# Performance work log

Measured on AMD Instinct MI355X. Metric: run time of the kernel, lower is better.

Reference implementation:

```python
import jax, jax.numpy as jnp
import numpy as np

D_MODEL, D_FF, N_EXPERTS, TOP_K = 512, 2048, 8, 2


def setup_inputs() -> dict:
    key = jax.random.key(0)
    ks = jax.random.split(key, 7)
    B, S = 2, 2048
    x = jax.random.normal(ks[0], (B, S, D_MODEL), dtype=jnp.float32)
    s1 = 1.0 / np.sqrt(D_MODEL)
    s2 = 1.0 / np.sqrt(D_FF)
    Wg = jax.random.normal(ks[1], (D_MODEL, N_EXPERTS), dtype=jnp.float32) * s1
    bg = jnp.zeros((N_EXPERTS,), dtype=jnp.float32)
    W1 = jax.random.normal(ks[2], (N_EXPERTS, D_MODEL, D_FF), dtype=jnp.float32) * s1
    b1 = jax.random.normal(ks[3], (N_EXPERTS, D_FF), dtype=jnp.float32) * s1
    W2 = jax.random.normal(ks[4], (N_EXPERTS, D_FF, D_MODEL), dtype=jnp.float32) * s2
    b2 = jax.random.normal(ks[5], (N_EXPERTS, D_MODEL), dtype=jnp.float32) * s2
    return {"x": x, "Wg": Wg, "bg": bg, "W1": W1, "b1": b1, "W2": W2, "b2": b2}


def reference(x, Wg, bg, W1, b1, W2, b2):
    B, S, D = x.shape
    xt = x.reshape(B * S, D)  # [T, D]
    # gating
    gate_logits = xt @ Wg + bg                      # [T, E]
    gate_scores = jax.nn.softmax(gate_logits, axis=-1)
    topk_scores, topk_idx = jax.lax.top_k(gate_scores, TOP_K)  # [T, K]
    topk_scores = topk_scores / jnp.sum(topk_scores, axis=-1, keepdims=True)
    # combine weights per expert: [T, E]
    combine = jnp.sum(jax.nn.one_hot(topk_idx, N_EXPERTS, dtype=xt.dtype)
                      * topk_scores[..., None], axis=1)
    # dense per-expert MLP (exact GELU, dropout is identity in eval)
    h = jax.nn.gelu(jnp.einsum('td,edf->etf', xt, W1) + b1[:, None, :],
                    approximate=False)             # [E, T, F]
    expert_out = jnp.einsum('etf,efd->etd', h, W2) + b2[:, None, :]  # [E, T, D]
    out = jnp.einsum('te,etd->td', combine, expert_out)
    return out.reshape(B, S, D)
```

## Files before the change

kernel.cpp:

```cpp
#include <hip/hip_runtime.h>
#include <hip/hip_bf16.h>
#include <math.h>

#define D_MODEL 512
#define D_FF    2048
#define NEXP    8

using bf16x8 = __attribute__((ext_vector_type(8))) short;
using f32x4  = __attribute__((ext_vector_type(4))) float;

__device__ inline unsigned short f2bf(float x) {
    __hip_bfloat16 h = __float2bfloat16(x);
    unsigned short u; __builtin_memcpy(&u, &h, 2); return u;
}
__device__ inline unsigned pk(float a, float b) {
    return (unsigned)f2bf(a) | ((unsigned)f2bf(b) << 16);
}
__device__ inline float erf_fast(float x) {
    float ax = fabsf(x);
    float t  = 1.f / fmaf(0.3275911f, ax, 1.f);
    float p  = t * fmaf(t, fmaf(t, fmaf(t, fmaf(t, 1.061405429f, -1.453152027f),
                                        1.421413741f), -0.284496736f), 0.254829592f);
    float r  = 1.f - p * __expf(-ax * ax);
    return copysignf(r, x);
}
__device__ inline float gelu_exact(float v) {
    return 0.5f * v * (1.f + erf_fast(v * 0.70710678118654752f));
}
__device__ inline void gload_lds16(const void* g, void* l) {
    __builtin_amdgcn_global_load_lds(
        (const __attribute__((address_space(1))) unsigned int*)g,
        (__attribute__((address_space(3))) unsigned int*)l, 16, 0, 0);
}

__global__ __launch_bounds__(256) void gate_kernel(
    const float* __restrict__ x, const float* __restrict__ Wg,
    const float* __restrict__ bg,
    int2* __restrict__ tk_e, float2* __restrict__ tk_s,
    unsigned short* __restrict__ Xb, int T)
{
    int lane = threadIdx.x & 63;
    int w    = threadIdx.x >> 6;
    int t    = blockIdx.x * 4 + w;
    if (t >= T) return;

    const float* xr = x + (size_t)t * D_MODEL;
    unsigned short* xbr = Xb ? (Xb + (size_t)t * D_MODEL) : nullptr;
    float lg[NEXP];
#pragma unroll
    for (int e = 0; e < NEXP; e++) lg[e] = 0.f;

#pragma unroll
    for (int it = 0; it < D_MODEL / 64; it++) {
        int d = lane + 64 * it;
        float xv = xr[d];
        if (xbr) xbr[d] = f2bf(xv);
        const float* wr = Wg + (size_t)d * NEXP;
#pragma unroll
        for (int e = 0; e < NEXP; e++) lg[e] += xv * wr[e];
    }
#pragma unroll
    for (int off = 32; off > 0; off >>= 1) {
#pragma unroll
        for (int e = 0; e < NEXP; e++) lg[e] += __shfl_xor(lg[e], off, 64);
    }

    if (lane == 0) {
#pragma unroll
        for (int e = 0; e < NEXP; e++) lg[e] += bg[e];
        int e0 = 0;
#pragma unroll
        for (int e = 1; e < NEXP; e++) if (lg[e] > lg[e0]) e0 = e;
        int e1 = (e0 == 0) ? 1 : 0;
#pragma unroll
        for (int e = 0; e < NEXP; e++) if (e != e0 && lg[e] > lg[e1]) e1 = e;
        float s0 = 1.f / (1.f + expf(lg[e1] - lg[e0]));
        tk_e[t] = make_int2(e0, e1);
        tk_s[t] = make_float2(s0, 1.f - s0);
    }
}

__global__ __launch_bounds__(256) void route_kernel(
    const int2* __restrict__ tk_e, const float2* __restrict__ tk_s,
    int* __restrict__ counts, int* __restrict__ ltok, float* __restrict__ lsc,
    int2* __restrict__ tk_pos, int T)
{
    int t    = blockIdx.x * 256 + threadIdx.x;
    int lane = threadIdx.x & 63;
    bool valid = t < T;
    int2   es = valid ? tk_e[t] : make_int2(-1, -1);
    float2 ss = valid ? tk_s[t] : make_float2(0.f, 0.f);
    int ppos[2] = {0, 0};

#pragma unroll
    for (int slot = 0; slot < 2; slot++) {
        int   e = slot ? es.y : es.x;
        float s = slot ? ss.y : ss.x;
#pragma unroll
        for (int ex = 0; ex < NEXP; ex++) {
            unsigned long long m = __ballot(e == ex);
            if (m == 0ull) continue;
            int leader = __ffsll((long long)m) - 1;
            int base = 0;
            if (lane == leader) base = atomicAdd(&counts[ex], __popcll(m));
            base = __shfl(base, leader, 64);
            if (e == ex) {
                int pos = base + __popcll(m & ((1ull << lane) - 1ull));
                ltok[(size_t)ex * T + pos] = t;
                lsc [(size_t)ex * T + pos] = s;
                ppos[slot] = pos | (ex << 16);
            }
        }
    }
    if (valid) tk_pos[t] = make_int2(ppos[0], ppos[1]);
}

__global__ void prefix_kernel(const int* __restrict__ counts, int* __restrict__ offs)
{
    if (threadIdx.x == 0) {
        int acc = 0;
        for (int e = 0; e < NEXP; e++) { offs[e] = acc; acc += counts[e]; }
        offs[NEXP] = acc;
    }
}

__global__ __launch_bounds__(256) void tcvt_kernel(
    const float* __restrict__ src, unsigned short* __restrict__ dst, int R, int C)
{
    __shared__ unsigned short tile[64][72];
    int e  = blockIdx.z;
    int r0 = blockIdx.y * 64, c0 = blockIdx.x * 64;
    const float* s = src + ((size_t)e * R + r0) * C + c0;
    unsigned short* d = dst + ((size_t)e * C + c0) * R + r0;
    int t = threadIdx.x;
#pragma unroll
    for (int i = 0; i < 4; i++) {
        int idx = t + 256 * i;
        int r = idx >> 4, c4 = (idx & 15) * 4;
        float4 v = *(const float4*)(s + (size_t)r * C + c4);
        tile[c4    ][r] = f2bf(v.x);
        tile[c4 + 1][r] = f2bf(v.y);
        tile[c4 + 2][r] = f2bf(v.z);
        tile[c4 + 3][r] = f2bf(v.w);
    }
    __syncthreads();
#pragma unroll
    for (int i = 0; i < 2; i++) {
        int idx = t + 256 * i;
        int c = idx >> 3, q = idx & 7;
        uint4 v = *(const uint4*)(&tile[c][q * 8]);
        *(uint4*)(d + (size_t)c * R + q * 8) = v;
    }
}

__global__ __launch_bounds__(512, 4) void moe_gemm1(
    const unsigned short* __restrict__ Xb,
    const unsigned short* __restrict__ W1t, const float* __restrict__ b1,
    const int* __restrict__ counts, const int* __restrict__ offs,
    const int* __restrict__ ltok,
    unsigned short* __restrict__ Hg, int T)
{
    int e = blockIdx.x;
    int n = counts[e];
    int mbase = blockIdx.y * 128;
    if (mbase >= n) return;
    int fb = blockIdx.z * 128;
    int off = offs[e];

    __shared__ __align__(16) unsigned char SB[2][16384];
    __shared__ int toks_s[128];

    int tid = threadIdx.x, lane = tid & 63, wid = tid >> 6;
    int wr = wid & 3, wc = wid >> 2;

    if (tid < 128) {
        int idx = mbase + tid; if (idx > n - 1) idx = n - 1;
        toks_s[tid] = ltok[(size_t)e * T + idx];
    }
    __syncthreads();

    const unsigned short* W1te = W1t + (size_t)e * D_FF * D_MODEL;
    int c = lane & 7, rsub = lane >> 3;

    const char* aptr[2]; const char* bptr[2]; int soff[2];
#pragma unroll
    for (int j = 0; j < 2; j++) {
        int r  = j * 64 + wid * 8 + rsub;
        int sc = c ^ (r & 7);
        aptr[j] = (const char*)(Xb + (size_t)toks_s[r] * D_MODEL) + sc * 16;
        bptr[j] = (const char*)(W1te + (size_t)(fb + r) * D_MODEL) + sc * 16;
        soff[j] = (j * 64 + wid * 8) * 128;
    }

    f32x4 acc[2][4];
#pragma unroll
    for (int i = 0; i < 2; i++)
#pragma unroll
        for (int j = 0; j < 4; j++) acc[i][j] = (f32x4){0.f, 0.f, 0.f, 0.f};

    for (int kc = 0; kc < D_MODEL; kc += 64) {
#pragma unroll
        for (int j = 0; j < 2; j++) gload_lds16(aptr[j] + kc * 2, SB[0] + soff[j]);
#pragma unroll
        for (int j = 0; j < 2; j++) gload_lds16(bptr[j] + kc * 2, SB[1] + soff[j]);
        __syncthreads();

#pragma unroll
        for (int ks = 0; ks < 2; ks++) {
            bf16x8 av[2], bv[4];
            int kbyte = ks * 64 + ((lane >> 4) * 16);
#pragma unroll
            for (int i = 0; i < 2; i++) {
                int row = wr * 32 + i * 16 + (lane & 15);
                av[i] = *(const bf16x8*)(SB[0] + row * 128 + (kbyte ^ ((row & 7) << 4)));
            }
#pragma unroll
            for (int j = 0; j < 4; j++) {
                int fr = wc * 64 + j * 16 + (lane & 15);
                bv[j] = *(const bf16x8*)(SB[1] + fr * 128 + (kbyte ^ ((fr & 7) << 4)));
            }
#pragma unroll
            for (int i = 0; i < 2; i++)
#pragma unroll
                for (int j = 0; j < 4; j++)
                    acc[i][j] = __builtin_amdgcn_mfma_f32_16x16x32_bf16(av[i], bv[j], acc[i][j], 0, 0, 0);
        }
        __syncthreads();
    }

    char* Eb = (char*)&SB[0][0];
    const float* b1e = b1 + (size_t)e * D_FF;
#pragma unroll
    for (int j = 0; j < 4; j++) {
        int col = wc * 64 + j * 16 + (lane & 15);
        float b1v = b1e[fb + col];
#pragma unroll
        for (int i = 0; i < 2; i++) {
#pragma unroll
            for (int r = 0; r < 4; r++) {
                int row = wr * 32 + i * 16 + (lane >> 4) * 4 + r;
                float v = gelu_exact(acc[i][j][r] + b1v);
                *(unsigned short*)(Eb + row * 256 + ((col * 2) ^ ((row & 7) << 4))) = f2bf(v);
            }
        }
    }
    __syncthreads();
#pragma unroll
    for (int k = 0; k < 4; k++) {
        int idx = tid + 512 * k;
        int row = idx >> 4, ch = idx & 15;
        if (mbase + row < n) {
            uint4 v = *(const uint4*)(Eb + row * 256 + ((ch * 16) ^ ((row & 7) << 4)));
            *(uint4*)(Hg + (size_t)(off + mbase + row) * D_FF + fb + ch * 8) = v;
        }
    }
}

__global__ __launch_bounds__(512, 4) void moe_gemm2_og(
    const unsigned short* __restrict__ Hg,
    const unsigned short* __restrict__ W2t, const float* __restrict__ b2,
    const int* __restrict__ counts, const int* __restrict__ offs,
    const int* __restrict__ ltok, const float* __restrict__ lsc,
    float* __restrict__ Og, int T)
{
    int e = blockIdx.x;
    int n = counts[e];
    int mbase = blockIdx.y * 128;
    if (mbase >= n) return;
    int nb = blockIdx.z & 3, kb = blockIdx.z >> 2;
    int db = nb * 128;
    int off = offs[e];

    __shared__ __align__(16) unsigned char SB[2][16384];
    __shared__ float scs_s[128];

    int tid = threadIdx.x, lane = tid & 63, wid = tid >> 6;
    int wr = wid & 3, wc = wid >> 2;

    if (tid < 128) {
        int idx = mbase + tid; if (idx > n - 1) idx = n - 1;
        scs_s[tid] = lsc[(size_t)e * T + idx];
    }
    __syncthreads();

    const unsigned short* W2te = W2t + (size_t)e * D_MODEL * D_FF;
    int c = lane & 7, rsub = lane >> 3;

    const char* aptr[2]; const char* bptr[2]; int soff[2];
#pragma unroll
    for (int j = 0; j < 2; j++) {
        int r = j * 64 + wid * 8 + rsub;
        int srow = mbase + r; if (srow > n - 1) srow = n - 1;
        int sc = c ^ (r & 7);
        aptr[j] = (const char*)(Hg + (size_t)(off + srow) * D_FF) + sc * 16;
        bptr[j] = (const char*)(W2te + (size_t)(db + r) * D_FF) + sc * 16;
        soff[j] = (j * 64 + wid * 8) * 128;
    }

    f32x4 acc[2][4];
#pragma unroll
    for (int i = 0; i < 2; i++)
#pragma unroll
        for (int j = 0; j < 4; j++) acc[i][j] = (f32x4){0.f, 0.f, 0.f, 0.f};

    int kbase = kb * 1024;
    for (int kc = 0; kc < 1024; kc += 64) {
        int kabs = kbase + kc;
#pragma unroll
        for (int j = 0; j < 2; j++) gload_lds16(aptr[j] + kabs * 2, SB[0] + soff[j]);
#pragma unroll
        for (int j = 0; j < 2; j++) gload_lds16(bptr[j] + kabs * 2, SB[1] + soff[j]);
        __syncthreads();

#pragma unroll
        for (int ks = 0; ks < 2; ks++) {
            bf16x8 av[2], bv[4];
            int kbyte = ks * 64 + ((lane >> 4) * 16);
#pragma unroll
            for (int i = 0; i < 2; i++) {
                int row = wr * 32 + i * 16 + (lane & 15);
                av[i] = *(const bf16x8*)(SB[0] + row * 128 + (kbyte ^ ((row & 7) << 4)));
            }
#pragma unroll
            for (int j = 0; j < 4; j++) {
                int dr = wc * 64 + j * 16 + (lane & 15);
                bv[j] = *(const bf16x8*)(SB[1] + dr * 128 + (kbyte ^ ((dr & 7) << 4)));
            }
#pragma unroll
            for (int i = 0; i < 2; i++)
#pragma unroll
                for (int j = 0; j < 4; j++)
                    acc[i][j] = __builtin_amdgcn_mfma_f32_16x16x32_bf16(av[i], bv[j], acc[i][j], 0, 0, 0);
        }
        __syncthreads();
    }

    float* Ogk = Og + (size_t)kb * (2 * T) * D_MODEL;
#pragma unroll
    for (int j = 0; j < 4; j++) {
        int dg = db + wc * 64 + j * 16 + (lane & 15);
        float b2v = (kb == 0) ? b2[(size_t)e * D_MODEL + dg] : 0.f;
#pragma unroll
        for (int i = 0; i < 2; i++) {
#pragma unroll
            for (int r = 0; r < 4; r++) {
                int rowm = wr * 32 + i * 16 + (lane >> 4) * 4 + r;
                if (mbase + rowm < n) {
                    float s = scs_s[rowm];
                    Ogk[(size_t)(off + mbase + rowm) * D_MODEL + dg] = s * (acc[i][j][r] + b2v);
                }
            }
        }
    }
}

__global__ __launch_bounds__(256) void combine_kernel(
    const float* __restrict__ Og, const int* __restrict__ offs,
    const int2* __restrict__ tk_pos, float* __restrict__ out, int T)
{
    int w = threadIdx.x >> 6, lane = threadIdx.x & 63;
    int t = blockIdx.x * 4 + w;
    if (t >= T) return;
    int2 p = tk_pos[t];
    int sA = offs[p.x >> 16] + (p.x & 0xffff);
    int sB = offs[p.y >> 16] + (p.y & 0xffff);
    size_t S = (size_t)(2 * T) * D_MODEL;
    const float4* r0 = (const float4*)(Og + (size_t)sA * D_MODEL);
    const float4* r1 = (const float4*)(Og + S + (size_t)sA * D_MODEL);
    const float4* r2 = (const float4*)(Og + (size_t)sB * D_MODEL);
    const float4* r3 = (const float4*)(Og + S + (size_t)sB * D_MODEL);
    float4* o = (float4*)(out + (size_t)t * D_MODEL);
#pragma unroll
    for (int i = 0; i < 2; i++) {
        int idx = lane + 64 * i;
        float4 a = r0[idx], b = r1[idx], cc = r2[idx], d = r3[idx];
        o[idx] = make_float4(a.x + b.x + cc.x + d.x, a.y + b.y + cc.y + d.y,
                             a.z + b.z + cc.z + d.z, a.w + b.w + cc.w + d.w);
    }
}

__global__ __launch_bounds__(256, 4) void moe_gemm2(
    const unsigned short* __restrict__ Hg,
    const unsigned short* __restrict__ W2t, const float* __restrict__ b2,
    const int* __restrict__ counts, const int* __restrict__ offs,
    const int* __restrict__ ltok, const float* __restrict__ lsc,
    float* __restrict__ out, int T)
{
    int e = blockIdx.x;
    int n = counts[e];
    int mbase = blockIdx.y * 128;
    if (mbase >= n) return;
    int nb = blockIdx.z & 3, kb = blockIdx.z >> 2;
    int db = nb * 128;
    int off = offs[e];

    __shared__ __align__(16) unsigned char HsB[128 * 128];
    __shared__ __align__(16) unsigned char WsB[128 * 128];
    __shared__ int   toks_s[128];
    __shared__ float scs_s[128];

    int tid = threadIdx.x, lane = tid & 63, w = tid >> 6;
    int wr = w & 1, wc = w >> 1;

    if (tid < 128) {
        int idx = mbase + tid; if (idx > n - 1) idx = n - 1;
        toks_s[tid] = ltok[(size_t)e * T + idx];
        scs_s [tid] = lsc [(size_t)e * T + idx];
    }
    __syncthreads();

    const unsigned short* W2te = W2t + (size_t)e * D_MODEL * D_FF;
    int c = lane & 7, rsub = lane >> 3;

    const char* aptr[4]; const char* bptr[4]; int soff[4];
#pragma unroll
    for (int j = 0; j < 4; j++) {
        int r = j * 32 + w * 8 + rsub;
        int srow = mbase + r; if (srow > n - 1) srow = n - 1;
        int sc = c ^ (r & 7);
        aptr[j] = (const char*)(Hg + (size_t)(off + srow) * D_FF) + sc * 16;
        bptr[j] = (const char*)(W2te + (size_t)(db + r) * D_FF) + sc * 16;
        soff[j] = (j * 32 + w * 8) * 128;
    }

    f32x4 acc[4][4];
#pragma unroll
    for (int i = 0; i < 4; i++)
#pragma unroll
        for (int j = 0; j < 4; j++) acc[i][j] = (f32x4){0.f, 0.f, 0.f, 0.f};

    int kbase = kb * 1024;
    for (int kc = 0; kc < 1024; kc += 64) {
        int kabs = kbase + kc;
#pragma unroll
        for (int j = 0; j < 4; j++) gload_lds16(aptr[j] + kabs * 2, HsB + soff[j]);
#pragma unroll
        for (int j = 0; j < 4; j++) gload_lds16(bptr[j] + kabs * 2, WsB + soff[j]);
        __syncthreads();

#pragma unroll
        for (int ks = 0; ks < 2; ks++) {
            bf16x8 av[4], bv[4];
            int kbyte = ks * 64 + ((lane >> 4) * 16);
#pragma unroll
            for (int i = 0; i < 4; i++) {
                int row = wr * 64 + i * 16 + (lane & 15);
                av[i] = *(const bf16x8*)(HsB + row * 128 + (kbyte ^ ((row & 7) << 4)));
            }
#pragma unroll
            for (int j = 0; j < 4; j++) {
                int dr = wc * 64 + j * 16 + (lane & 15);
                bv[j] = *(const bf16x8*)(WsB + dr * 128 + (kbyte ^ ((dr & 7) << 4)));
            }
#pragma unroll
            for (int i = 0; i < 4; i++)
#pragma unroll
                for (int j = 0; j < 4; j++)
                    acc[i][j] = __builtin_amdgcn_mfma_f32_16x16x32_bf16(av[i], bv[j], acc[i][j], 0, 0, 0);
        }
        __syncthreads();
    }

#pragma unroll
    for (int j = 0; j < 4; j++) {
        int dg = db + wc * 64 + j * 16 + (lane & 15);
        float b2v = (kb == 0) ? b2[(size_t)e * D_MODEL + dg] : 0.f;
#pragma unroll
        for (int i = 0; i < 4; i++) {
#pragma unroll
            for (int r = 0; r < 4; r++) {
                int rowm = wr * 64 + i * 16 + (lane >> 4) * 4 + r;
                if (mbase + rowm < n) {
                    float s = scs_s[rowm];
                    int tok = toks_s[rowm];
                    atomicAdd(out + (size_t)tok * D_MODEL + dg, s * (acc[i][j][r] + b2v));
                }
            }
        }
    }
}

__global__ __launch_bounds__(512, 2) void moe_gemm1_rs(
    const float* __restrict__ x,
    const float* __restrict__ W1, const float* __restrict__ b1,
    const int* __restrict__ counts, const int* __restrict__ offs,
    const int* __restrict__ ltok,
    unsigned short* __restrict__ Hg, int T)
{
    int e = blockIdx.x;
    int n = counts[e];
    int mbase = blockIdx.y * 128;
    if (mbase >= n) return;
    int fb = blockIdx.z * 256;
    int off = offs[e];

    __shared__ __align__(16) unsigned char XsB[128 * 128];
    __shared__ __align__(16) unsigned char WtB[256 * 128];
    __shared__ int toks_s[128];

    int tid  = threadIdx.x;
    int lane = tid & 63;
    int w    = tid >> 6;
    int wr   = w & 1, wc = w >> 1;

    if (tid < 128) {
        int idx = mbase + tid; if (idx > n - 1) idx = n - 1;
        toks_s[tid] = ltok[(size_t)e * T + idx];
    }
    __syncthreads();

    const float* W1e = W1 + (size_t)e * D_MODEL * D_FF;

    f32x4 acc[4][4];
#pragma unroll
    for (int i = 0; i < 4; i++)
#pragma unroll
        for (int j = 0; j < 4; j++) acc[i][j] = (f32x4){0.f, 0.f, 0.f, 0.f};

    int fcol = tid & 255, khalf = tid >> 8;
    const float* w1col = W1e + fb + fcol;

    for (int kc = 0; kc < D_MODEL; kc += 64) {
#pragma unroll
        for (int i = 0; i < 4; i++) {
            int idx = tid + 512 * i;
            int r = idx >> 4, c4 = idx & 15;
            const float4 v = *(const float4*)(x + (size_t)toks_s[r] * D_MODEL + kc + c4 * 4);
            *(uint2*)(XsB + r * 128 + ((c4 * 8) ^ ((r & 7) << 4))) =
                make_uint2(pk(v.x, v.y), pk(v.z, v.w));
        }
#pragma unroll
        for (int j = 0; j < 8; j++) {
            int q  = khalf * 8 + j;
            int k0 = kc + q * 4;
            float a0 = w1col[(size_t)(k0    ) * D_FF];
            float a1 = w1col[(size_t)(k0 + 1) * D_FF];
            float a2 = w1col[(size_t)(k0 + 2) * D_FF];
            float a3 = w1col[(size_t)(k0 + 3) * D_FF];
            *(uint2*)(WtB + fcol * 128 + ((q * 8) ^ ((fcol & 7) << 4))) =
                make_uint2(pk(a0, a1), pk(a2, a3));
        }
        __syncthreads();

#pragma unroll
        for (int ks = 0; ks < 2; ks++) {
            bf16x8 av[4], bv[4];
            int kbyte = ks * 64 + ((lane >> 4) * 16);
#pragma unroll
            for (int i = 0; i < 4; i++) {
                int row = wr * 64 + i * 16 + (lane & 15);
                av[i] = *(const bf16x8*)(XsB + row * 128 + (kbyte ^ ((row & 7) << 4)));
            }
#pragma unroll
            for (int j = 0; j < 4; j++) {
                int fr = wc * 64 + j * 16 + (lane & 15);
                bv[j] = *(const bf16x8*)(WtB + fr * 128 + (kbyte ^ ((fr & 7) << 4)));
            }
#pragma unroll
            for (int i = 0; i < 4; i++)
#pragma unroll
                for (int j = 0; j < 4; j++)
                    acc[i][j] = __builtin_amdgcn_mfma_f32_16x16x32_bf16(av[i], bv[j], acc[i][j], 0, 0, 0);
        }
        __syncthreads();
    }

    const float* b1e = b1 + (size_t)e * D_FF;
#pragma unroll
    for (int j = 0; j < 4; j++) {
        int fg = fb + wc * 64 + j * 16 + (lane & 15);
        float b1v = b1e[fg];
#pragma unroll
        for (int i = 0; i < 4; i++) {
#pragma unroll
            for (int r = 0; r < 4; r++) {
                int rowm = wr * 64 + i * 16 + (lane >> 4) * 4 + r;
                if (mbase + rowm < n) {
                    float v = gelu_exact(acc[i][j][r] + b1v);
                    Hg[(size_t)(off + mbase + rowm) * D_FF + fg] = f2bf(v);
                }
            }
        }
    }
}

__global__ __launch_bounds__(512, 2) void moe_gemm2_rs(
    const unsigned short* __restrict__ Hg,
    const float* __restrict__ W2, const float* __restrict__ b2,
    const int* __restrict__ counts, const int* __restrict__ offs,
    const int* __restrict__ ltok, const float* __restrict__ lsc,
    float* __restrict__ out, int T)
{
    int e = blockIdx.x;
    int n = counts[e];
    int mbase = blockIdx.y * 128;
    if (mbase >= n) return;
    int nb = blockIdx.z & 1, kb = blockIdx.z >> 1;
    int db = nb * 256;
    int off = offs[e];

    __shared__ __align__(16) unsigned char HsB[128 * 128];
    __shared__ __align__(16) unsigned char WtB[256 * 128];
    __shared__ int   toks_s[128];
    __shared__ float scs_s[128];

    int tid  = threadIdx.x;
    int lane = tid & 63;
    int w    = tid >> 6;
    int wr   = w & 1, wc = w >> 1;

    if (tid < 128) {
        int idx = mbase + tid; if (idx > n - 1) idx = n - 1;
        toks_s[tid] = ltok[(size_t)e * T + idx];
        scs_s [tid] = lsc [(size_t)e * T + idx];
    }
    __syncthreads();

    const float* W2e = W2 + (size_t)e * D_FF * D_MODEL;

    f32x4 acc[4][4];
#pragma unroll
    for (int i = 0; i < 4; i++)
#pragma unroll
        for (int j = 0; j < 4; j++) acc[i][j] = (f32x4){0.f, 0.f, 0.f, 0.f};

    int dcol = tid & 255, khalf = tid >> 8;
    const float* w2col = W2e + db + dcol;

    for (int kc = 0; kc < 1024; kc += 64) {
        int kabs = kb * 1024 + kc;
#pragma unroll
        for (int i = 0; i < 2; i++) {
            int idx = tid + 512 * i;
            int r = idx >> 3, c16 = idx & 7;
            int srow = mbase + r; if (srow > n - 1) srow = n - 1;
            const uint4 v = *(const uint4*)(Hg + (size_t)(off + srow) * D_FF + kabs + c16 * 8);
            *(uint4*)(HsB + r * 128 + ((c16 * 16) ^ ((r & 7) << 4))) = v;
        }
#pragma unroll
        for (int j = 0; j < 8; j++) {
            int q  = khalf * 8 + j;
            int k0 = kabs + q * 4;
            float a0 = w2col[(size_t)(k0    ) * D_MODEL];
            float a1 = w2col[(size_t)(k0 + 1) * D_MODEL];
            float a2 = w2col[(size_t)(k0 + 2) * D_MODEL];
            float a3 = w2col[(size_t)(k0 + 3) * D_MODEL];
            *(uint2*)(WtB + dcol * 128 + ((q * 8) ^ ((dcol & 7) << 4))) =
                make_uint2(pk(a0, a1), pk(a2, a3));
        }
        __syncthreads();

#pragma unroll
        for (int ks = 0; ks < 2; ks++) {
            bf16x8 av[4], bv[4];
            int kbyte = ks * 64 + ((lane >> 4) * 16);
#pragma unroll
            for (int i = 0; i < 4; i++) {
                int row = wr * 64 + i * 16 + (lane & 15);
                av[i] = *(const bf16x8*)(HsB + row * 128 + (kbyte ^ ((row & 7) << 4)));
            }
#pragma unroll
            for (int j = 0; j < 4; j++) {
                int dr = wc * 64 + j * 16 + (lane & 15);
                bv[j] = *(const bf16x8*)(WtB + dr * 128 + (kbyte ^ ((dr & 7) << 4)));
            }
#pragma unroll
            for (int i = 0; i < 4; i++)
#pragma unroll
                for (int j = 0; j < 4; j++)
                    acc[i][j] = __builtin_amdgcn_mfma_f32_16x16x32_bf16(av[i], bv[j], acc[i][j], 0, 0, 0);
        }
        __syncthreads();
    }

#pragma unroll
    for (int j = 0; j < 4; j++) {
        int dg = db + wc * 64 + j * 16 + (lane & 15);
        float b2v = (kb == 0) ? b2[(size_t)e * D_MODEL + dg] : 0.f;
#pragma unroll
        for (int i = 0; i < 4; i++) {
#pragma unroll
            for (int r = 0; r < 4; r++) {
                int rowm = wr * 64 + i * 16 + (lane >> 4) * 4 + r;
                if (mbase + rowm < n) {
                    float s = scs_s[rowm];
                    int tok = toks_s[rowm];
                    atomicAdd(out + (size_t)tok * D_MODEL + dg, s * (acc[i][j][r] + b2v));
                }
            }
        }
    }
}

extern "C" void kernel_launch(void* const* d_in, const int* in_sizes, int n_in,
                              void* d_out, int out_size, void* d_ws, size_t ws_size,
                              hipStream_t stream)
{
    const float* x  = (const float*)d_in[0];
    const float* Wg = (const float*)d_in[1];
    const float* bg = (const float*)d_in[2];
    const float* W1 = (const float*)d_in[3];
    const float* b1 = (const float*)d_in[4];
    const float* W2 = (const float*)d_in[5];
    const float* b2 = (const float*)d_in[6];
    float* out = (float*)d_out;
    int T = in_sizes[0] / D_MODEL;

    int*    counts = (int*)d_ws;
    int*    offs   = (int*)((char*)d_ws + 64);
    int*    ltok   = (int*)((char*)d_ws + 256);
    float*  lsc    = (float*)((char*)d_ws + 256 + (size_t)NEXP * T * sizeof(int));
    int2*   tk_e   = (int2*)((char*)d_ws + 256 + (size_t)2 * NEXP * T * sizeof(int));
    float2* tk_s   = (float2*)((char*)tk_e + (size_t)T * sizeof(int2));
    int2*   tk_pos = (int2*)((char*)tk_s + (size_t)T * sizeof(float2));

    const size_t Hoff   = 512 * 1024;
    const size_t Hbytes = (size_t)2 * T * D_FF * sizeof(unsigned short);
    const size_t Xoff   = Hoff + Hbytes;
    const size_t Xbytes = (size_t)T * D_MODEL * sizeof(unsigned short);
    const size_t W1off  = Xoff + Xbytes;
    const size_t Wbytes = (size_t)NEXP * D_MODEL * D_FF * sizeof(unsigned short);
    const size_t W2off  = W1off + Wbytes;
    const size_t Ogoff  = W2off + Wbytes;
    const size_t Ogbytes = (size_t)2 * (2 * T) * D_MODEL * sizeof(float);
    const size_t need_og   = Ogoff + Ogbytes + 4096;
    const size_t need_full = W2off + Wbytes + 4096;
    const size_t need_r2   = Hoff + Hbytes + 4096;

    bool og   = ws_size >= need_og;
    bool full = ws_size >= need_full;
    unsigned short* Xb = full ? (unsigned short*)((char*)d_ws + Xoff) : nullptr;

    hipMemsetAsync(d_ws, 0, 256, stream);
    if (!og)
        hipMemsetAsync(d_out, 0, (size_t)out_size * sizeof(float), stream);

    gate_kernel<<<dim3((T + 3) / 4), dim3(256), 0, stream>>>(
        x, Wg, bg, tk_e, tk_s, Xb, T);
    route_kernel<<<dim3((T + 255) / 256), dim3(256), 0, stream>>>(
        tk_e, tk_s, counts, ltok, lsc, tk_pos, T);
    prefix_kernel<<<dim3(1), dim3(64), 0, stream>>>(counts, offs);

    if (full) {
        unsigned short* Hg  = (unsigned short*)((char*)d_ws + Hoff);
        unsigned short* W1t = (unsigned short*)((char*)d_ws + W1off);
        unsigned short* W2t = (unsigned short*)((char*)d_ws + W2off);

        tcvt_kernel<<<dim3(D_FF / 64, D_MODEL / 64, NEXP), dim3(256), 0, stream>>>(
            W1, W1t, D_MODEL, D_FF);
        tcvt_kernel<<<dim3(D_MODEL / 64, D_FF / 64, NEXP), dim3(256), 0, stream>>>(
            W2, W2t, D_FF, D_MODEL);

        moe_gemm1<<<dim3(NEXP, (T + 127) / 128, D_FF / 128), dim3(512), 0, stream>>>(
            Xb, W1t, b1, counts, offs, ltok, Hg, T);

        if (og) {
            float* Og = (float*)((char*)d_ws + Ogoff);
            moe_gemm2_og<<<dim3(NEXP, (T + 127) / 128, 8), dim3(512), 0, stream>>>(
                Hg, W2t, b2, counts, offs, ltok, lsc, Og, T);
            combine_kernel<<<dim3((T + 3) / 4), dim3(256), 0, stream>>>(
                Og, offs, tk_pos, out, T);
        } else {
            moe_gemm2<<<dim3(NEXP, (T + 127) / 128, 8), dim3(256), 0, stream>>>(
                Hg, W2t, b2, counts, offs, ltok, lsc, out, T);
        }
    } else if (ws_size >= need_r2) {
        unsigned short* Hg = (unsigned short*)((char*)d_ws + Hoff);
        moe_gemm1_rs<<<dim3(NEXP, (T + 127) / 128, D_FF / 256), dim3(512), 0, stream>>>(
            x, W1, b1, counts, offs, ltok, Hg, T);
        moe_gemm2_rs<<<dim3(NEXP, (T + 127) / 128, 4), dim3(512), 0, stream>>>(
            Hg, W2, b2, counts, offs, ltok, lsc, out, T);
    }
}
```

Baseline: 139.6 us.

## Enlarge MoE GEMM tiles to 256 rows and double-buffer LDS staging

Both expert GEMM kernels move to larger block tiles: gemm1 goes to 256x256 and gemm2 to 256x128. LDS staging is now double-buffered, so the next K-chunk's global-to-LDS loads are issued before the current chunk's MFMAs, and each K step needs one barrier instead of two. The aim is more operand reuse per loaded byte and overlap of memory latency with compute. In exchange, occupancy drops to one block per CU, LDS use grows to 128KB and 96KB, accumulator register pressure rises, and with per-expert token counts around 1024 there are fewer blocks to fill the GPU.

Measured after the change: 166.4 us. +19.2%, slower.

```diff
diff --git a/kernel.cpp b/kernel.cpp
--- a/kernel.cpp
+++ b/kernel.cpp
@@ -153,7 +153,7 @@
     }
 }
 
-__global__ __launch_bounds__(512, 4) void moe_gemm1(
+__global__ __launch_bounds__(512, 1) void moe_gemm1(
     const unsigned short* __restrict__ Xb,
     const unsigned short* __restrict__ W1t, const float* __restrict__ b1,
     const int* __restrict__ counts, const int* __restrict__ offs,
@@ -162,18 +162,18 @@
 {
     int e = blockIdx.x;
     int n = counts[e];
-    int mbase = blockIdx.y * 128;
+    int mbase = blockIdx.y * 256;
     if (mbase >= n) return;
-    int fb = blockIdx.z * 128;
+    int fb = blockIdx.z * 256;
     int off = offs[e];
 
-    __shared__ __align__(16) unsigned char SB[2][16384];
-    __shared__ int toks_s[128];
+    __shared__ __align__(16) unsigned char SB[2][65536];
+    __shared__ int toks_s[256];
 
     int tid = threadIdx.x, lane = tid & 63, wid = tid >> 6;
-    int wr = wid & 3, wc = wid >> 2;
-
-    if (tid < 128) {
+    int wr = wid >> 2, wc = wid & 3;
+
+    if (tid < 256) {
         int idx = mbase + tid; if (idx > n - 1) idx = n - 1;
         toks_s[tid] = ltok[(size_t)e * T + idx];
     }
@@ -182,9 +182,9 @@
     const unsigned short* W1te = W1t + (size_t)e * D_FF * D_MODEL;
     int c = lane & 7, rsub = lane >> 3;
 
-    const char* aptr[2]; const char* bptr[2]; int soff[2];
-#pragma unroll
-    for (int j = 0; j < 2; j++) {
+    const char* aptr[4]; const char* bptr[4]; int soff[4];
+#pragma unroll
+    for (int j = 0; j < 4; j++) {
         int r  = j * 64 + wid * 8 + rsub;
         int sc = c ^ (r & 7);
         aptr[j] = (const char*)(Xb + (size_t)toks_s[r] * D_MODEL) + sc * 16;
@@ -192,41 +192,54 @@
         soff[j] = (j * 64 + wid * 8) * 128;
     }
 
-    f32x4 acc[2][4];
-#pragma unroll
-    for (int i = 0; i < 2; i++)
+    f32x4 acc[8][4];
+#pragma unroll
+    for (int i = 0; i < 8; i++)
 #pragma unroll
         for (int j = 0; j < 4; j++) acc[i][j] = (f32x4){0.f, 0.f, 0.f, 0.f};
 
-    for (int kc = 0; kc < D_MODEL; kc += 64) {
-#pragma unroll
-        for (int j = 0; j < 2; j++) gload_lds16(aptr[j] + kc * 2, SB[0] + soff[j]);
-#pragma unroll
-        for (int j = 0; j < 2; j++) gload_lds16(bptr[j] + kc * 2, SB[1] + soff[j]);
+#define STG1(buf, kc)                                                          \
+    do {                                                                       \
+        _Pragma("unroll")                                                      \
+        for (int j = 0; j < 4; j++) gload_lds16(aptr[j] + (kc) * 2, SB[buf] + soff[j]);          \
+        _Pragma("unroll")                                                      \
+        for (int j = 0; j < 4; j++) gload_lds16(bptr[j] + (kc) * 2, SB[buf] + 32768 + soff[j]);  \
+    } while (0)
+
+    STG1(0, 0);
+    __syncthreads();
+#pragma unroll 2
+    for (int kt = 0; kt < 8; ++kt) {
+        int b = kt & 1;
+        if (kt < 7) STG1(b ^ 1, (kt + 1) * 64);
+        const unsigned char* As = SB[b];
+        const unsigned char* Bs = SB[b] + 32768;
+
+        bf16x8 bv[4][2];
+#pragma unroll
+        for (int j = 0; j < 4; j++) {
+            int fr = wc * 64 + j * 16 + (lane & 15);
+#pragma unroll
+            for (int ks = 0; ks < 2; ks++)
+                bv[j][ks] = *(const bf16x8*)(Bs + fr * 128 +
+                    ((ks * 64 + (lane >> 4) * 16) ^ ((fr & 7) << 4)));
+        }
+#pragma unroll
+        for (int i = 0; i < 8; i++) {
+            int row = wr * 128 + i * 16 + (lane & 15);
+            bf16x8 av0 = *(const bf16x8*)(As + row * 128 +
+                (((lane >> 4) * 16)      ^ ((row & 7) << 4)));
+            bf16x8 av1 = *(const bf16x8*)(As + row * 128 +
+                ((64 + (lane >> 4) * 16) ^ ((row & 7) << 4)));
+#pragma unroll
+            for (int j = 0; j < 4; j++) {
+                acc[i][j] = __builtin_amdgcn_mfma_f32_16x16x32_bf16(av0, bv[j][0], acc[i][j], 0, 0, 0);
+                acc[i][j] = __builtin_amdgcn_mfma_f32_16x16x32_bf16(av1, bv[j][1], acc[i][j], 0, 0, 0);
+            }
+        }
         __syncthreads();
-
-#pragma unroll
-        for (int ks = 0; ks < 2; ks++) {
-            bf16x8 av[2], bv[4];
-            int kbyte = ks * 64 + ((lane >> 4) * 16);
-#pragma unroll
-            for (int i = 0; i < 2; i++) {
-                int row = wr * 32 + i * 16 + (lane & 15);
-                av[i] = *(const bf16x8*)(SB[0] + row * 128 + (kbyte ^ ((row & 7) << 4)));
-            }
-#pragma unroll
-            for (int j = 0; j < 4; j++) {
-                int fr = wc * 64 + j * 16 + (lane & 15);
-                bv[j] = *(const bf16x8*)(SB[1] + fr * 128 + (kbyte ^ ((fr & 7) << 4)));
-            }
-#pragma unroll
-            for (int i = 0; i < 2; i++)
-#pragma unroll
-                for (int j = 0; j < 4; j++)
-                    acc[i][j] = __builtin_amdgcn_mfma_f32_16x16x32_bf16(av[i], bv[j], acc[i][j], 0, 0, 0);
-        }
-        __syncthreads();
-    }
+    }
+#undef STG1
 
     char* Eb = (char*)&SB[0][0];
     const float* b1e = b1 + (size_t)e * D_FF;
@@ -235,28 +248,28 @@
         int col = wc * 64 + j * 16 + (lane & 15);
         float b1v = b1e[fb + col];
 #pragma unroll
-        for (int i = 0; i < 2; i++) {
+        for (int i = 0; i < 8; i++) {
 #pragma unroll
             for (int r = 0; r < 4; r++) {
-                int row = wr * 32 + i * 16 + (lane >> 4) * 4 + r;
+                int row = wr * 128 + i * 16 + (lane >> 4) * 4 + r;
                 float v = gelu_exact(acc[i][j][r] + b1v);
-                *(unsigned short*)(Eb + row * 256 + ((col * 2) ^ ((row & 7) << 4))) = f2bf(v);
+                *(unsigned short*)(Eb + row * 512 + ((col * 2) ^ ((row & 7) << 4))) = f2bf(v);
             }
         }
     }
     __syncthreads();
 #pragma unroll
-    for (int k = 0; k < 4; k++) {
+    for (int k = 0; k < 16; k++) {
         int idx = tid + 512 * k;
-        int row = idx >> 4, ch = idx & 15;
+        int row = idx >> 5, ch = idx & 31;
         if (mbase + row < n) {
-            uint4 v = *(const uint4*)(Eb + row * 256 + ((ch * 16) ^ ((row & 7) << 4)));
+            uint4 v = *(const uint4*)(Eb + row * 512 + ((ch * 16) ^ ((row & 7) << 4)));
             *(uint4*)(Hg + (size_t)(off + mbase + row) * D_FF + fb + ch * 8) = v;
         }
     }
 }
 
-__global__ __launch_bounds__(512, 4) void moe_gemm2_og(
+__global__ __launch_bounds__(512, 1) void moe_gemm2_og(
     const unsigned short* __restrict__ Hg,
     const unsigned short* __restrict__ W2t, const float* __restrict__ b2,
     const int* __restrict__ counts, const int* __restrict__ offs,
@@ -265,19 +278,19 @@
 {
     int e = blockIdx.x;
     int n = counts[e];
-    int mbase = blockIdx.y * 128;
+    int mbase = blockIdx.y * 256;
     if (mbase >= n) return;
     int nb = blockIdx.z & 3, kb = blockIdx.z >> 2;
     int db = nb * 128;
     int off = offs[e];
 
-    __shared__ __align__(16) unsigned char SB[2][16384];
-    __shared__ float scs_s[128];
+    __shared__ __align__(16) unsigned char SB[2][49152];
+    __shared__ float scs_s[256];
 
     int tid = threadIdx.x, lane = tid & 63, wid = tid >> 6;
-    int wr = wid & 3, wc = wid >> 2;
-
-    if (tid < 128) {
+    int wr = wid >> 2, wc = wid & 3;
+
+    if (tid < 256) {
         int idx = mbase + tid; if (idx > n - 1) idx = n - 1;
         scs_s[tid] = lsc[(size_t)e * T + idx];
     }
@@ -286,65 +299,84 @@
     const unsigned short* W2te = W2t + (size_t)e * D_MODEL * D_FF;
     int c = lane & 7, rsub = lane >> 3;
 
-    const char* aptr[2]; const char* bptr[2]; int soff[2];
-#pragma unroll
-    for (int j = 0; j < 2; j++) {
+    const char* aptr[4]; int soffA[4];
+#pragma unroll
+    for (int j = 0; j < 4; j++) {
         int r = j * 64 + wid * 8 + rsub;
         int srow = mbase + r; if (srow > n - 1) srow = n - 1;
         int sc = c ^ (r & 7);
-        aptr[j] = (const char*)(Hg + (size_t)(off + srow) * D_FF) + sc * 16;
-        bptr[j] = (const char*)(W2te + (size_t)(db + r) * D_FF) + sc * 16;
-        soff[j] = (j * 64 + wid * 8) * 128;
-    }
-
-    f32x4 acc[2][4];
-#pragma unroll
-    for (int i = 0; i < 2; i++)
-#pragma unroll
-        for (int j = 0; j < 4; j++) acc[i][j] = (f32x4){0.f, 0.f, 0.f, 0.f};
+        aptr[j]  = (const char*)(Hg + (size_t)(off + srow) * D_FF) + sc * 16;
+        soffA[j] = (j * 64 + wid * 8) * 128;
+    }
+    const char* bptr[2]; int soffB[2];
+#pragma unroll
+    for (int j = 0; j < 2; j++) {
+        int r  = j * 64 + wid * 8 + rsub;
+        int sc = c ^ (r & 7);
+        bptr[j]  = (const char*)(W2te + (size_t)(db + r) * D_FF) + sc * 16;
+        soffB[j] = (j * 64 + wid * 8) * 128;
+    }
+
+    f32x4 acc[8][2];
+#pragma unroll
+    for (int i = 0; i < 8; i++)
+#pragma unroll
+        for (int j = 0; j < 2; j++) acc[i][j] = (f32x4){0.f, 0.f, 0.f, 0.f};
+
+#define STG2(buf, kc)                                                          \
+    do {                                                                       \
+        _Pragma("unroll")                                                      \
+        for (int j = 0; j < 4; j++) gload_lds16(aptr[j] + (kc) * 2, SB[buf] + soffA[j]);         \
+        _Pragma("unroll")                                                      \
+        for (int j = 0; j < 2; j++) gload_lds16(bptr[j] + (kc) * 2, SB[buf] + 32768 + soffB[j]); \
+    } while (0)
 
     int kbase = kb * 1024;
-    for (int kc = 0; kc < 1024; kc += 64) {
-        int kabs = kbase + kc;
-#pragma unroll
-        for (int j = 0; j < 2; j++) gload_lds16(aptr[j] + kabs * 2, SB[0] + soff[j]);
-#pragma unroll
-        for (int j = 0; j < 2; j++) gload_lds16(bptr[j] + kabs * 2, SB[1] + soff[j]);
+    STG2(0, kbase);
+    __syncthreads();
+#pragma unroll 2
+    for (int kt = 0; kt < 16; ++kt) {
+        int b = kt & 1;
+        if (kt < 15) STG2(b ^ 1, kbase + (kt + 1) * 64);
+        const unsigned char* As = SB[b];
+        const unsigned char* Bs = SB[b] + 32768;
+
+        bf16x8 bv[2][2];
+#pragma unroll
+        for (int j = 0; j < 2; j++) {
+            int fr = wc * 32 + j * 16 + (lane & 15);
+#pragma unroll
+            for (int ks = 0; ks < 2; ks++)
+                bv[j][ks] = *(const bf16x8*)(Bs + fr * 128 +
+                    ((ks * 64 + (lane >> 4) * 16) ^ ((fr & 7) << 4)));
+        }
+#pragma unroll
+        for (int i = 0; i < 8; i++) {
+            int row = wr * 128 + i * 16 + (lane & 15);
+            bf16x8 av0 = *(const bf16x8*)(As + row * 128 +
+                (((lane >> 4) * 16)      ^ ((row & 7) << 4)));
+            bf16x8 av1 = *(const bf16x8*)(As + row * 128 +
+                ((64 + (lane >> 4) * 16) ^ ((row & 7) << 4)));
+#pragma unroll
+            for (int j = 0; j < 2; j++) {
+                acc[i][j] = __builtin_amdgcn_mfma_f32_16x16x32_bf16(av0, bv[j][0], acc[i][j], 0, 0, 0);
+                acc[i][j] = __builtin_amdgcn_mfma_f32_16x16x32_bf16(av1, bv[j][1], acc[i][j], 0, 0, 0);
+            }
+        }
         __syncthreads();
-
-#pragma unroll
-        for (int ks = 0; ks < 2; ks++) {
-            bf16x8 av[2], bv[4];
-            int kbyte = ks * 64 + ((lane >> 4) * 16);
-#pragma unroll
-            for (int i = 0; i < 2; i++) {
-                int row = wr * 32 + i * 16 + (lane & 15);
-                av[i] = *(const bf16x8*)(SB[0] + row * 128 + (kbyte ^ ((row & 7) << 4)));
-            }
-#pragma unroll
-            for (int j = 0; j < 4; j++) {
-                int dr = wc * 64 + j * 16 + (lane & 15);
-                bv[j] = *(const bf16x8*)(SB[1] + dr * 128 + (kbyte ^ ((dr & 7) << 4)));
-            }
-#pragma unroll
-            for (int i = 0; i < 2; i++)
-#pragma unroll
-                for (int j = 0; j < 4; j++)
-                    acc[i][j] = __builtin_amdgcn_mfma_f32_16x16x32_bf16(av[i], bv[j], acc[i][j], 0, 0, 0);
-        }
-        __syncthreads();
-    }
+    }
+#undef STG2
 
     float* Ogk = Og + (size_t)kb * (2 * T) * D_MODEL;
 #pragma unroll
-    for (int j = 0; j < 4; j++) {
-        int dg = db + wc * 64 + j * 16 + (lane & 15);
+    for (int j = 0; j < 2; j++) {
+        int dg = db + wc * 32 + j * 16 + (lane & 15);
         float b2v = (kb == 0) ? b2[(size_t)e * D_MODEL + dg] : 0.f;
 #pragma unroll
-        for (int i = 0; i < 2; i++) {
+        for (int i = 0; i < 8; i++) {
 #pragma unroll
             for (int r = 0; r < 4; r++) {
-                int rowm = wr * 32 + i * 16 + (lane >> 4) * 4 + r;
+                int rowm = wr * 128 + i * 16 + (lane >> 4) * 4 + r;
                 if (mbase + rowm < n) {
                     float s = scs_s[rowm];
                     Ogk[(size_t)(off + mbase + rowm) * D_MODEL + dg] = s * (acc[i][j][r] + b2v);
@@ -751,12 +783,12 @@
         tcvt_kernel<<<dim3(D_MODEL / 64, D_FF / 64, NEXP), dim3(256), 0, stream>>>(
             W2, W2t, D_FF, D_MODEL);
 
-        moe_gemm1<<<dim3(NEXP, (T + 127) / 128, D_FF / 128), dim3(512), 0, stream>>>(
+        moe_gemm1<<<dim3(NEXP, (T + 255) / 256, D_FF / 256), dim3(512), 0, stream>>>(
             Xb, W1t, b1, counts, offs, ltok, Hg, T);
 
         if (og) {
             float* Og = (float*)((char*)d_ws + Ogoff);
-            moe_gemm2_og<<<dim3(NEXP, (T + 127) / 128, 8), dim3(512), 0, stream>>>(
+            moe_gemm2_og<<<dim3(NEXP, (T + 255) / 256, 8), dim3(512), 0, stream>>>(
                 Hg, W2t, b2, counts, offs, ltok, lsc, Og, T);
             combine_kernel<<<dim3((T + 3) / 4), dim3(256), 0, stream>>>(
                 Og, offs, tk_pos, out, T);
```
